# Optimization experiments

Measured on AMD Instinct MI355X. Metric: run time of the kernel, lower is better.

The kernel has to match this reference:

```python
import jax, jax.numpy as jnp
import numpy as np

B, D, N, F = 2048, 512, 100000, 64
NEG = -1000000.0


def setup_inputs() -> dict:
    key = jax.random.key(0)
    k1, k2, k3, k4 = jax.random.split(key, 4)
    q = jax.random.normal(k1, (B, D), dtype=jnp.float32)
    rhs = jax.random.normal(k2, (D, N), dtype=jnp.float32)
    queries = jax.random.randint(k3, (B, 3), 0, N, dtype=jnp.int64)
    filter_idx = jax.random.randint(k4, (B, F), 0, N, dtype=jnp.int64)
    return {"q": q, "rhs": rhs, "queries": queries, "filter_idx": filter_idx}


def reference(q, rhs, queries, filter_idx):
    # targets[i] = score of the true triple = q[i] . rhs[:, true_rhs[i]]
    true_rhs = queries[:, 2]                         # [B]
    targets = jnp.einsum('bd,bd->b', q, rhs[:, true_rhs].T)  # [B]

    scores = q @ rhs                                  # [B, N]

    # filtered ranking: mask out known true tails + the query's own tail
    rows = jnp.arange(scores.shape[0])[:, None]       # [B, 1]
    scores = scores.at[rows, filter_idx].set(NEG)
    scores = scores.at[jnp.arange(scores.shape[0]), true_rhs].set(NEG)

    # rank = 1 + number of candidates scoring >= the true triple
    ranks = 1.0 + jnp.sum((scores >= targets[:, None]).astype(jnp.float32), axis=1)
    return ranks
```

## Files before the change

kernel.cpp:

```cpp
#include <hip/hip_runtime.h>
#include <hip/hip_bf16.h>

#define B_ 2048
#define D_ 512
#define N_ 100000
#define F_ 64
#define NEGV (-1000000.0f)

typedef __bf16 bfx8 __attribute__((ext_vector_type(8)));
typedef float f32x4 __attribute__((ext_vector_type(4)));
typedef unsigned short u16x8 __attribute__((ext_vector_type(8)));

static __device__ __forceinline__ unsigned short f2bf(float f) {
  unsigned u = __float_as_uint(f);
  unsigned r = (u + 0x7fffu + ((u >> 16) & 1u)) >> 16;
  return (unsigned short)r;
}
static __device__ __forceinline__ float bf2f(unsigned short u) {
  return __uint_as_float(((unsigned)u) << 16);
}

static __device__ __forceinline__ void async_copy16(const void* g, void* l) {
  __builtin_amdgcn_global_load_lds((const __attribute__((address_space(1))) void*)g,
                                   (__attribute__((address_space(3))) void*)l, 16, 0, 0);
}

__global__ void targets_convert(const float* __restrict__ q, const float* __restrict__ rhs,
                                const int* __restrict__ queries, float* __restrict__ targets,
                                float* __restrict__ out, unsigned short* __restrict__ qb) {
  __shared__ float wsum[4];
  int b = blockIdx.x;
  int tid = threadIdx.x, lane = tid & 63, w = tid >> 6;
  int p = queries[b * 3 + 2];
  float2 v = ((const float2*)(q + (size_t)b * D_))[tid];
  ushort2 o; o.x = f2bf(v.x); o.y = f2bf(v.y);
  ((ushort2*)(qb + (size_t)b * D_))[tid] = o;
  float s = v.x * rhs[(size_t)(2 * tid) * N_ + p] + v.y * rhs[(size_t)(2 * tid + 1) * N_ + p];
  for (int off = 32; off; off >>= 1) s += __shfl_down(s, off, 64);
  if (lane == 0) wsum[w] = s;
  __syncthreads();
  if (tid == 0) {
    targets[b] = wsum[0] + wsum[1] + wsum[2] + wsum[3];
    out[b] = 1.0f;
  }
}

__global__ void transpose_rhs(const float* __restrict__ rhs, unsigned short* __restrict__ rt) {
  __shared__ float tile[32][260];
  int n0 = blockIdx.x * 256, d0 = blockIdx.y * 32;
  int tid = threadIdx.x;
  if (n0 + 256 <= N_) {
#pragma unroll
    for (int p = 0; p < 8; ++p) {
      int e = p * 256 + tid;
      int d = e >> 6, c4 = e & 63;
      float4 v = *(const float4*)(rhs + (size_t)(d0 + d) * N_ + n0 + c4 * 4);
      *(float4*)&tile[d][c4 * 4] = v;
    }
    __syncthreads();
#pragma unroll
    for (int p = 0; p < 8; ++p) {
      int e = p * 256 + tid;
      int n = e >> 3, dg = e & 7;
      ushort4 o;
      o.x = f2bf(tile[dg * 4 + 0][n]);
      o.y = f2bf(tile[dg * 4 + 1][n]);
      o.z = f2bf(tile[dg * 4 + 2][n]);
      o.w = f2bf(tile[dg * 4 + 3][n]);
      *(ushort4*)(rt + (size_t)(n0 + n) * D_ + d0 + dg * 4) = o;
    }
  } else {
#pragma unroll
    for (int p = 0; p < 8; ++p) {
      int e = p * 256 + tid;
      int d = e >> 6, c4 = e & 63;
      if (n0 + c4 * 4 + 3 < N_) {
        float4 v = *(const float4*)(rhs + (size_t)(d0 + d) * N_ + n0 + c4 * 4);
        *(float4*)&tile[d][c4 * 4] = v;
      }
    }
    __syncthreads();
#pragma unroll
    for (int p = 0; p < 8; ++p) {
      int e = p * 256 + tid;
      int n = e >> 3, dg = e & 7;
      if (n0 + n < N_) {
        ushort4 o;
        o.x = f2bf(tile[dg * 4 + 0][n]);
        o.y = f2bf(tile[dg * 4 + 1][n]);
        o.z = f2bf(tile[dg * 4 + 2][n]);
        o.w = f2bf(tile[dg * 4 + 3][n]);
        *(ushort4*)(rt + (size_t)(n0 + n) * D_ + d0 + dg * 4) = o;
      }
    }
  }
}

__global__ void __launch_bounds__(256) gemm_count(
    const unsigned short* __restrict__ qb,
    const unsigned short* __restrict__ rt,
    const float* __restrict__ targets,
    float* __restrict__ out) {
  __shared__ unsigned short As[2][128 * 32];
  __shared__ unsigned short Bs[2][128 * 32];
  __shared__ float sT[128];
  __shared__ int cnt2[2][128];

  int tid = threadIdx.x;
  int m0 = blockIdx.x * 128;
  int n0 = blockIdx.y * 128;

  if (tid < 128) sT[tid] = targets[m0 + tid];

  int w = tid >> 6, lane = tid & 63;
  int mw = (w & 1) * 64, nw = (w >> 1) * 64;
  int quad = lane >> 4, l16 = lane & 15;

  int c0 = tid, c1 = 256 + tid;
  int am0 = c0 >> 2, aj0 = (c0 & 3) * 8;
  int am1 = c1 >> 2, aj1 = (c1 & 3) * 8;
  int bn0g = n0 + am0; if (bn0g > N_ - 1) bn0g = N_ - 1;
  int bn1g = n0 + am1; if (bn1g > N_ - 1) bn1g = N_ - 1;
  const unsigned short* agp0 = qb + (size_t)(m0 + am0) * D_ + aj0;
  const unsigned short* agp1 = qb + (size_t)(m0 + am1) * D_ + aj1;
  const unsigned short* bgp0 = rt + (size_t)bn0g * D_ + aj0;
  const unsigned short* bgp1 = rt + (size_t)bn1g * D_ + aj1;

  f32x4 acc[4][4];
  f32x4 z = {0.f, 0.f, 0.f, 0.f};
#pragma unroll
  for (int i = 0; i < 4; ++i)
#pragma unroll
    for (int j = 0; j < 4; ++j) acc[i][j] = z;

  async_copy16(agp0, &As[0][c0 * 8]);
  async_copy16(agp1, &As[0][c1 * 8]);
  async_copy16(bgp0, &Bs[0][c0 * 8]);
  async_copy16(bgp1, &Bs[0][c1 * 8]);

  for (int kt = 0; kt < 16; ++kt) {
    int buf = kt & 1;
    __syncthreads();
    if (kt + 1 < 16) {
      int nb = 1 - buf, k1 = (kt + 1) * 32;
      async_copy16(agp0 + k1, &As[nb][c0 * 8]);
      async_copy16(agp1 + k1, &As[nb][c1 * 8]);
      async_copy16(bgp0 + k1, &Bs[nb][c0 * 8]);
      async_copy16(bgp1 + k1, &Bs[nb][c1 * 8]);
    }

    bfx8 a[4], b[4];
#pragma unroll
    for (int mi = 0; mi < 4; ++mi) {
      int m = mw + mi * 16 + l16;
      u16x8 au = *(const u16x8*)(&As[buf][m * 32 + quad * 8]);
      a[mi] = __builtin_bit_cast(bfx8, au);
    }
#pragma unroll
    for (int ni = 0; ni < 4; ++ni) {
      int n = nw + ni * 16 + l16;
      u16x8 bu = *(const u16x8*)(&Bs[buf][n * 32 + quad * 8]);
      b[ni] = __builtin_bit_cast(bfx8, bu);
    }
#pragma unroll
    for (int mi = 0; mi < 4; ++mi)
#pragma unroll
      for (int ni = 0; ni < 4; ++ni)
        acc[mi][ni] = __builtin_amdgcn_mfma_f32_16x16x32_bf16(a[mi], b[ni], acc[mi][ni], 0, 0, 0);
  }

#pragma unroll
  for (int mi = 0; mi < 4; ++mi) {
#pragma unroll
    for (int reg = 0; reg < 4; ++reg) {
      int rl = mw + mi * 16 + quad * 4 + reg;
      float t = sT[rl];
      int c = 0;
#pragma unroll
      for (int ni = 0; ni < 4; ++ni) {
        int col = n0 + nw + ni * 16 + l16;
        if (col < N_ && acc[mi][ni][reg] >= t) c++;
      }
      c += __shfl_xor(c, 1, 64);
      c += __shfl_xor(c, 2, 64);
      c += __shfl_xor(c, 4, 64);
      c += __shfl_xor(c, 8, 64);
      if (l16 == 0) cnt2[w >> 1][rl] = c;
    }
  }
  __syncthreads();
  if (tid < 128) {
    int tot = cnt2[0][tid] + cnt2[1][tid];
    if (tot) atomicAdd(&out[m0 + tid], (float)tot);
  }
}

__global__ void __launch_bounds__(1024) corrections(
    const unsigned short* __restrict__ qb,
    const unsigned short* __restrict__ rt,
    const int* __restrict__ queries,
    const int* __restrict__ filt,
    const float* __restrict__ targets,
    float* __restrict__ out) {
  int b = blockIdx.x;
  int tid = threadIdx.x;
  int w = tid >> 6, lane = tid & 63;
  __shared__ int idx[F_ + 1];
  __shared__ unsigned char uq[F_ + 1];
  if (tid <= F_) idx[tid] = (tid < F_) ? filt[b * F_ + tid] : queries[b * 3 + 2];
  __syncthreads();
  if (tid <= F_) {
    int p = idx[tid];
    bool u = true;
    for (int j = 0; j < tid; ++j)
      if (idx[j] == p) u = false;
    uq[tid] = u;
  }
  __syncthreads();
  float t = targets[b];
  float corr = 0.f;
  u16x8 qv = ((const u16x8*)(qb + (size_t)b * D_))[lane];
  for (int ii = w; ii <= F_; ii += 16) {
    if (!uq[ii]) continue;
    int p = idx[ii];
    u16x8 rv = ((const u16x8*)(rt + (size_t)p * D_))[lane];
    float s = 0.f;
#pragma unroll
    for (int j = 0; j < 8; ++j) s += bf2f(qv[j]) * bf2f(rv[j]);
    for (int off = 32; off; off >>= 1) s += __shfl_down(s, off, 64);
    if (lane == 0)
      corr += (NEGV >= t ? 1.f : 0.f) - (s >= t ? 1.f : 0.f);
  }
  if (lane == 0 && corr != 0.f) atomicAdd(&out[b], corr);
}

__global__ void targets_init(const float* __restrict__ q, const float* __restrict__ rhs,
                             const int* __restrict__ queries, float* __restrict__ targets,
                             float* __restrict__ out) {
  __shared__ float wsum[4];
  int b = blockIdx.x;
  int tid = threadIdx.x, lane = tid & 63, w = tid >> 6;
  int p = queries[b * 3 + 2];
  float s = 0.f;
  for (int d = tid; d < D_; d += 256) s += q[b * D_ + d] * rhs[(size_t)d * N_ + p];
  for (int off = 32; off; off >>= 1) s += __shfl_down(s, off, 64);
  if (lane == 0) wsum[w] = s;
  __syncthreads();
  if (tid == 0) {
    targets[b] = wsum[0] + wsum[1] + wsum[2] + wsum[3];
    out[b] = 1.0f;
  }
}

__global__ void fallback_count(const float* __restrict__ q, const float* __restrict__ rhs,
                               const int* __restrict__ queries, const int* __restrict__ filt,
                               const float* __restrict__ targets, float* __restrict__ out) {
  int b = blockIdx.y;
  int n = blockIdx.x * 256 + threadIdx.x;
  __shared__ float qs[D_];
  __shared__ int idx[F_ + 1];
  __shared__ int cnt;
  for (int d = threadIdx.x; d < D_; d += 256) qs[d] = q[b * D_ + d];
  if (threadIdx.x < F_) idx[threadIdx.x] = filt[b * F_ + threadIdx.x];
  if (threadIdx.x == F_) idx[F_] = queries[b * 3 + 2];
  if (threadIdx.x == 0) cnt = 0;
  __syncthreads();
  if (n < N_) {
    float t = targets[b];
    float s = 0.f;
    for (int d = 0; d < D_; ++d) s += qs[d] * rhs[(size_t)d * N_ + n];
    bool member = false;
    for (int j = 0; j <= F_; ++j)
      if (idx[j] == n) member = true;
    float sv = member ? NEGV : s;
    if (sv >= t) atomicAdd(&cnt, 1);
  }
  __syncthreads();
  if (threadIdx.x == 0 && cnt) atomicAdd(&out[b], (float)cnt);
}

extern "C" void kernel_launch(void* const* d_in, const int* in_sizes, int n_in,
                              void* d_out, int out_size, void* d_ws, size_t ws_size,
                              hipStream_t stream) {
  const float* q = (const float*)d_in[0];
  const float* rhs = (const float*)d_in[1];
  const int* queries = (const int*)d_in[2];
  const int* filt = (const int*)d_in[3];
  float* out = (float*)d_out;

  char* wsb = (char*)d_ws;
  float* targets = (float*)wsb;
  unsigned short* qb = (unsigned short*)(wsb + 8192);
  unsigned short* rt = (unsigned short*)(wsb + 8192 + (size_t)B_ * D_ * 2);
  size_t need = 8192 + (size_t)B_ * D_ * 2 + (size_t)N_ * D_ * 2;

  if (ws_size >= need) {
    targets_convert<<<B_, 256, 0, stream>>>(q, rhs, queries, targets, out, qb);
    transpose_rhs<<<dim3((N_ + 255) / 256, D_ / 32), 256, 0, stream>>>(rhs, rt);
    gemm_count<<<dim3(B_ / 128, (N_ + 127) / 128), 256, 0, stream>>>(qb, rt, targets, out);
    corrections<<<B_, 1024, 0, stream>>>(qb, rt, queries, filt, targets, out);
  } else {
    targets_init<<<B_, 256, 0, stream>>>(q, rhs, queries, targets, out);
    fallback_count<<<dim3((N_ + 255) / 256, B_), 256, 0, stream>>>(q, rhs, queries, filt, targets, out);
  }
}
```

Before: 636.0 us.

## Fuse filter masking into GEMM-count epilogue via per-tile bitmask

Removes the separate corrections kernel and instead builds, per 64x128 output tile, a shared-memory bitmask of filtered and true-tail columns. The GEMM epilogue then skips masked columns when counting. The tile shrinks to 64 rows with 128 threads (2 waves). Each block now scans all 64x64 filter indices for its rows, so every one of the many tiles rereads the filter list, and the smaller blocks halve A reuse per block. One behavioural difference: masked entries are now never counted, whereas the old correction added one count when NEG >= target.

```diff
diff --git a/kernel.cpp b/kernel.cpp
--- a/kernel.cpp
+++ b/kernel.cpp
@@ -15,9 +15,6 @@
   unsigned u = __float_as_uint(f);
   unsigned r = (u + 0x7fffu + ((u >> 16) & 1u)) >> 16;
   return (unsigned short)r;
-}
-static __device__ __forceinline__ float bf2f(unsigned short u) {
-  return __uint_as_float(((unsigned)u) << 16);
 }
 
 static __device__ __forceinline__ void async_copy16(const void* g, void* l) {
@@ -96,142 +93,130 @@
   }
 }
 
-__global__ void __launch_bounds__(256) gemm_count(
-    const unsigned short* __restrict__ qb,
-    const unsigned short* __restrict__ rt,
-    const float* __restrict__ targets,
-    float* __restrict__ out) {
-  __shared__ unsigned short As[2][128 * 32];
-  __shared__ unsigned short Bs[2][128 * 32];
-  __shared__ float sT[128];
-  __shared__ int cnt2[2][128];
-
-  int tid = threadIdx.x;
-  int m0 = blockIdx.x * 128;
-  int n0 = blockIdx.y * 128;
-
-  if (tid < 128) sT[tid] = targets[m0 + tid];
-
-  int w = tid >> 6, lane = tid & 63;
-  int mw = (w & 1) * 64, nw = (w >> 1) * 64;
-  int quad = lane >> 4, l16 = lane & 15;
-
-  int c0 = tid, c1 = 256 + tid;
-  int am0 = c0 >> 2, aj0 = (c0 & 3) * 8;
-  int am1 = c1 >> 2, aj1 = (c1 & 3) * 8;
-  int bn0g = n0 + am0; if (bn0g > N_ - 1) bn0g = N_ - 1;
-  int bn1g = n0 + am1; if (bn1g > N_ - 1) bn1g = N_ - 1;
-  const unsigned short* agp0 = qb + (size_t)(m0 + am0) * D_ + aj0;
-  const unsigned short* agp1 = qb + (size_t)(m0 + am1) * D_ + aj1;
-  const unsigned short* bgp0 = rt + (size_t)bn0g * D_ + aj0;
-  const unsigned short* bgp1 = rt + (size_t)bn1g * D_ + aj1;
-
-  f32x4 acc[4][4];
-  f32x4 z = {0.f, 0.f, 0.f, 0.f};
-#pragma unroll
-  for (int i = 0; i < 4; ++i)
-#pragma unroll
-    for (int j = 0; j < 4; ++j) acc[i][j] = z;
-
-  async_copy16(agp0, &As[0][c0 * 8]);
-  async_copy16(agp1, &As[0][c1 * 8]);
-  async_copy16(bgp0, &Bs[0][c0 * 8]);
-  async_copy16(bgp1, &Bs[0][c1 * 8]);
-
-  for (int kt = 0; kt < 16; ++kt) {
-    int buf = kt & 1;
-    __syncthreads();
-    if (kt + 1 < 16) {
-      int nb = 1 - buf, k1 = (kt + 1) * 32;
-      async_copy16(agp0 + k1, &As[nb][c0 * 8]);
-      async_copy16(agp1 + k1, &As[nb][c1 * 8]);
-      async_copy16(bgp0 + k1, &Bs[nb][c0 * 8]);
-      async_copy16(bgp1 + k1, &Bs[nb][c1 * 8]);
-    }
-
-    bfx8 a[4], b[4];
-#pragma unroll
-    for (int mi = 0; mi < 4; ++mi) {
-      int m = mw + mi * 16 + l16;
-      u16x8 au = *(const u16x8*)(&As[buf][m * 32 + quad * 8]);
-      a[mi] = __builtin_bit_cast(bfx8, au);
-    }
-#pragma unroll
-    for (int ni = 0; ni < 4; ++ni) {
-      int n = nw + ni * 16 + l16;
-      u16x8 bu = *(const u16x8*)(&Bs[buf][n * 32 + quad * 8]);
-      b[ni] = __builtin_bit_cast(bfx8, bu);
-    }
-#pragma unroll
-    for (int mi = 0; mi < 4; ++mi)
-#pragma unroll
-      for (int ni = 0; ni < 4; ++ni)
-        acc[mi][ni] = __builtin_amdgcn_mfma_f32_16x16x32_bf16(a[mi], b[ni], acc[mi][ni], 0, 0, 0);
-  }
-
-#pragma unroll
-  for (int mi = 0; mi < 4; ++mi) {
-#pragma unroll
-    for (int reg = 0; reg < 4; ++reg) {
-      int rl = mw + mi * 16 + quad * 4 + reg;
-      float t = sT[rl];
-      int c = 0;
-#pragma unroll
-      for (int ni = 0; ni < 4; ++ni) {
-        int col = n0 + nw + ni * 16 + l16;
-        if (col < N_ && acc[mi][ni][reg] >= t) c++;
-      }
-      c += __shfl_xor(c, 1, 64);
-      c += __shfl_xor(c, 2, 64);
-      c += __shfl_xor(c, 4, 64);
-      c += __shfl_xor(c, 8, 64);
-      if (l16 == 0) cnt2[w >> 1][rl] = c;
-    }
-  }
-  __syncthreads();
-  if (tid < 128) {
-    int tot = cnt2[0][tid] + cnt2[1][tid];
-    if (tot) atomicAdd(&out[m0 + tid], (float)tot);
-  }
-}
-
-__global__ void __launch_bounds__(1024) corrections(
+__global__ void __launch_bounds__(128) gemm_count(
     const unsigned short* __restrict__ qb,
     const unsigned short* __restrict__ rt,
     const int* __restrict__ queries,
     const int* __restrict__ filt,
     const float* __restrict__ targets,
     float* __restrict__ out) {
-  int b = blockIdx.x;
+  __shared__ unsigned short As[2][64 * 32];
+  __shared__ unsigned short Bs[2][128 * 32];
+  __shared__ float sT[64];
+  __shared__ int cnt2[2][64];
+  __shared__ unsigned bm[64][4];
+
   int tid = threadIdx.x;
+  int m0 = blockIdx.x * 64;
+  int n0 = blockIdx.y * 128;
+
   int w = tid >> 6, lane = tid & 63;
-  __shared__ int idx[F_ + 1];
-  __shared__ unsigned char uq[F_ + 1];
-  if (tid <= F_) idx[tid] = (tid < F_) ? filt[b * F_ + tid] : queries[b * 3 + 2];
-  __syncthreads();
-  if (tid <= F_) {
-    int p = idx[tid];
-    bool u = true;
-    for (int j = 0; j < tid; ++j)
-      if (idx[j] == p) u = false;
-    uq[tid] = u;
-  }
-  __syncthreads();
-  float t = targets[b];
-  float corr = 0.f;
-  u16x8 qv = ((const u16x8*)(qb + (size_t)b * D_))[lane];
-  for (int ii = w; ii <= F_; ii += 16) {
-    if (!uq[ii]) continue;
-    int p = idx[ii];
-    u16x8 rv = ((const u16x8*)(rt + (size_t)p * D_))[lane];
-    float s = 0.f;
-#pragma unroll
-    for (int j = 0; j < 8; ++j) s += bf2f(qv[j]) * bf2f(rv[j]);
-    for (int off = 32; off; off >>= 1) s += __shfl_down(s, off, 64);
-    if (lane == 0)
-      corr += (NEGV >= t ? 1.f : 0.f) - (s >= t ? 1.f : 0.f);
-  }
-  if (lane == 0 && corr != 0.f) atomicAdd(&out[b], corr);
+  int nw = w * 64;
+  int quad = lane >> 4, l16 = lane & 15;
+
+  if (tid < 64) sT[tid] = targets[m0 + tid];
+  ((unsigned*)bm)[tid] = 0;
+  ((unsigned*)bm)[128 + tid] = 0;
+
+  int ca0 = tid, ca1 = 128 + tid;
+  int am0 = ca0 >> 2, aj0 = (ca0 & 3) * 8;
+  int am1 = ca1 >> 2, aj1 = (ca1 & 3) * 8;
+  const unsigned short* agp0 = qb + (size_t)(m0 + am0) * D_ + aj0;
+  const unsigned short* agp1 = qb + (size_t)(m0 + am1) * D_ + aj1;
+  const unsigned short* bgp[4];
+  int cb[4];
+#pragma unroll
+  for (int i = 0; i < 4; ++i) {
+    int c = i * 128 + tid;
+    cb[i] = c;
+    int bn = c >> 2, bj = (c & 3) * 8;
+    int ng = n0 + bn; if (ng > N_ - 1) ng = N_ - 1;
+    bgp[i] = rt + (size_t)ng * D_ + bj;
+  }
+
+  f32x4 acc[4][4];
+  f32x4 z = {0.f, 0.f, 0.f, 0.f};
+#pragma unroll
+  for (int i = 0; i < 4; ++i)
+#pragma unroll
+    for (int j = 0; j < 4; ++j) acc[i][j] = z;
+
+  async_copy16(agp0, &As[0][ca0 * 8]);
+  async_copy16(agp1, &As[0][ca1 * 8]);
+#pragma unroll
+  for (int i = 0; i < 4; ++i) async_copy16(bgp[i], &Bs[0][cb[i] * 8]);
+
+  __syncthreads();
+
+  for (int i = tid; i < 64 * 64; i += 128) {
+    int r = i >> 6, j = i & 63;
+    int p = filt[(size_t)(m0 + r) * 64 + j];
+    unsigned o = (unsigned)(p - n0);
+    if (o < 128u) atomicOr(&bm[r][o >> 5], 1u << (o & 31));
+  }
+  if (tid < 64) {
+    int p = queries[(m0 + tid) * 3 + 2];
+    unsigned o = (unsigned)(p - n0);
+    if (o < 128u) atomicOr(&bm[tid][o >> 5], 1u << (o & 31));
+  }
+
+  for (int kt = 0; kt < 16; ++kt) {
+    int buf = kt & 1;
+    __syncthreads();
+    if (kt + 1 < 16) {
+      int nb = 1 - buf, k1 = (kt + 1) * 32;
+      async_copy16(agp0 + k1, &As[nb][ca0 * 8]);
+      async_copy16(agp1 + k1, &As[nb][ca1 * 8]);
+#pragma unroll
+      for (int i = 0; i < 4; ++i) async_copy16(bgp[i] + k1, &Bs[nb][cb[i] * 8]);
+    }
+
+    bfx8 a[4], b[4];
+#pragma unroll
+    for (int mi = 0; mi < 4; ++mi) {
+      int m = mi * 16 + l16;
+      u16x8 au = *(const u16x8*)(&As[buf][m * 32 + quad * 8]);
+      a[mi] = __builtin_bit_cast(bfx8, au);
+    }
+#pragma unroll
+    for (int ni = 0; ni < 4; ++ni) {
+      int n = nw + ni * 16 + l16;
+      u16x8 bu = *(const u16x8*)(&Bs[buf][n * 32 + quad * 8]);
+      b[ni] = __builtin_bit_cast(bfx8, bu);
+    }
+#pragma unroll
+    for (int mi = 0; mi < 4; ++mi)
+#pragma unroll
+      for (int ni = 0; ni < 4; ++ni)
+        acc[mi][ni] = __builtin_amdgcn_mfma_f32_16x16x32_bf16(a[mi], b[ni], acc[mi][ni], 0, 0, 0);
+  }
+
+#pragma unroll
+  for (int mi = 0; mi < 4; ++mi) {
+#pragma unroll
+    for (int reg = 0; reg < 4; ++reg) {
+      int rl = mi * 16 + quad * 4 + reg;
+      float t = sT[rl];
+      unsigned long long bmv = *(const unsigned long long*)&bm[rl][w * 2];
+      int c = 0;
+#pragma unroll
+      for (int ni = 0; ni < 4; ++ni) {
+        int o = ni * 16 + l16;
+        int col = n0 + nw + o;
+        if (col < N_ && !((bmv >> o) & 1ull) && acc[mi][ni][reg] >= t) c++;
+      }
+      c += __shfl_xor(c, 1, 64);
+      c += __shfl_xor(c, 2, 64);
+      c += __shfl_xor(c, 4, 64);
+      c += __shfl_xor(c, 8, 64);
+      if (l16 == 0) cnt2[w][rl] = c;
+    }
+  }
+  __syncthreads();
+  if (tid < 64) {
+    int tot = cnt2[0][tid] + cnt2[1][tid];
+    if (tot) atomicAdd(&out[m0 + tid], (float)tot);
+  }
 }
 
 __global__ void targets_init(const float* __restrict__ q, const float* __restrict__ rhs,
@@ -297,8 +282,7 @@
   if (ws_size >= need) {
     targets_convert<<<B_, 256, 0, stream>>>(q, rhs, queries, targets, out, qb);
     transpose_rhs<<<dim3((N_ + 255) / 256, D_ / 32), 256, 0, stream>>>(rhs, rt);
-    gemm_count<<<dim3(B_ / 128, (N_ + 127) / 128), 256, 0, stream>>>(qb, rt, targets, out);
-    corrections<<<B_, 1024, 0, stream>>>(qb, rt, queries, filt, targets, out);
+    gemm_count<<<dim3(B_ / 64, (N_ + 127) / 128), 128, 0, stream>>>(qb, rt, queries, filt, targets, out);
   } else {
     targets_init<<<B_, 256, 0, stream>>>(q, rhs, queries, targets, out);
     fallback_count<<<dim3((N_ + 255) / 256, B_), 256, 0, stream>>>(q, rhs, queries, filt, targets, out);
```

Result: slower. 798.5 us (+25.6%).

## Fuse filter masking into GEMM count via shared bitmask and swizzle tile order

Applied to the files above, without the earlier changes.

Removes the separate corrections kernel. Each GEMM tile now builds a per-row shared-memory bitmask of filtered and true-tail columns that fall inside its 128-column range, and skips those columns when counting scores at or above the target. The grid becomes 1D with a grouped mapping, so 8 neighbouring N-tiles run across all 16 M-tiles, which is meant to improve L2 reuse of the rhs tiles. The cost is that every block reads the full 128x64 filter slab for its M-tile and runs a pre-loop shared-atomic pass, which adds traffic and latency ahead of the MFMA loop.

```diff
diff --git a/kernel.cpp b/kernel.cpp
--- a/kernel.cpp
+++ b/kernel.cpp
@@ -6,6 +6,7 @@
 #define N_ 100000
 #define F_ 64
 #define NEGV (-1000000.0f)
+#define NT_ 782
 
 typedef __bf16 bfx8 __attribute__((ext_vector_type(8)));
 typedef float f32x4 __attribute__((ext_vector_type(4)));
@@ -15,9 +16,6 @@
   unsigned u = __float_as_uint(f);
   unsigned r = (u + 0x7fffu + ((u >> 16) & 1u)) >> 16;
   return (unsigned short)r;
-}
-static __device__ __forceinline__ float bf2f(unsigned short u) {
-  return __uint_as_float(((unsigned)u) << 16);
 }
 
 static __device__ __forceinline__ void async_copy16(const void* g, void* l) {
@@ -99,18 +97,29 @@
 __global__ void __launch_bounds__(256) gemm_count(
     const unsigned short* __restrict__ qb,
     const unsigned short* __restrict__ rt,
+    const int* __restrict__ queries,
+    const int* __restrict__ filt,
     const float* __restrict__ targets,
     float* __restrict__ out) {
   __shared__ unsigned short As[2][128 * 32];
   __shared__ unsigned short Bs[2][128 * 32];
   __shared__ float sT[128];
   __shared__ int cnt2[2][128];
+  __shared__ unsigned bm[128][4];
+
+  unsigned bid = blockIdx.x;
+  int c = bid & 7;
+  unsigned s = bid >> 3;
+  int m = s & 15, j = s >> 4;
+  int nt = j * 8 + c;
+  if (nt >= NT_) return;
+  int m0 = m * 128;
+  int n0 = nt * 128;
 
   int tid = threadIdx.x;
-  int m0 = blockIdx.x * 128;
-  int n0 = blockIdx.y * 128;
-
   if (tid < 128) sT[tid] = targets[m0 + tid];
+  ((unsigned*)bm)[tid] = 0;
+  ((unsigned*)bm)[256 + tid] = 0;
 
   int w = tid >> 6, lane = tid & 63;
   int mw = (w & 1) * 64, nw = (w >> 1) * 64;
@@ -131,12 +140,26 @@
 #pragma unroll
   for (int i = 0; i < 4; ++i)
 #pragma unroll
-    for (int j = 0; j < 4; ++j) acc[i][j] = z;
+    for (int jq = 0; jq < 4; ++jq) acc[i][jq] = z;
 
   async_copy16(agp0, &As[0][c0 * 8]);
   async_copy16(agp1, &As[0][c1 * 8]);
   async_copy16(bgp0, &Bs[0][c0 * 8]);
   async_copy16(bgp1, &Bs[0][c1 * 8]);
+
+  __syncthreads();
+
+  for (int i = tid; i < 128 * 64; i += 256) {
+    int r = i >> 6, f = i & 63;
+    int p = filt[(size_t)(m0 + r) * 64 + f];
+    unsigned o = (unsigned)(p - n0);
+    if (o < 128u) atomicOr(&bm[r][o >> 5], 1u << (o & 31));
+  }
+  if (tid < 128) {
+    int p = queries[(m0 + tid) * 3 + 2];
+    unsigned o = (unsigned)(p - n0);
+    if (o < 128u) atomicOr(&bm[tid][o >> 5], 1u << (o & 31));
+  }
 
   for (int kt = 0; kt < 16; ++kt) {
     int buf = kt & 1;
@@ -152,14 +175,14 @@
     bfx8 a[4], b[4];
 #pragma unroll
     for (int mi = 0; mi < 4; ++mi) {
-      int m = mw + mi * 16 + l16;
-      u16x8 au = *(const u16x8*)(&As[buf][m * 32 + quad * 8]);
+      int mm = mw + mi * 16 + l16;
+      u16x8 au = *(const u16x8*)(&As[buf][mm * 32 + quad * 8]);
       a[mi] = __builtin_bit_cast(bfx8, au);
     }
 #pragma unroll
     for (int ni = 0; ni < 4; ++ni) {
-      int n = nw + ni * 16 + l16;
-      u16x8 bu = *(const u16x8*)(&Bs[buf][n * 32 + quad * 8]);
+      int nn = nw + ni * 16 + l16;
+      u16x8 bu = *(const u16x8*)(&Bs[buf][nn * 32 + quad * 8]);
       b[ni] = __builtin_bit_cast(bfx8, bu);
     }
 #pragma unroll
@@ -175,17 +198,19 @@
     for (int reg = 0; reg < 4; ++reg) {
       int rl = mw + mi * 16 + quad * 4 + reg;
       float t = sT[rl];
-      int c = 0;
+      unsigned long long bmv = *(const unsigned long long*)&bm[rl][nw >> 5];
+      int cc = 0;
 #pragma unroll
       for (int ni = 0; ni < 4; ++ni) {
-        int col = n0 + nw + ni * 16 + l16;
-        if (col < N_ && acc[mi][ni][reg] >= t) c++;
+        int o = ni * 16 + l16;
+        int col = n0 + nw + o;
+        if (col < N_ && !((bmv >> o) & 1ull) && acc[mi][ni][reg] >= t) cc++;
       }
-      c += __shfl_xor(c, 1, 64);
-      c += __shfl_xor(c, 2, 64);
-      c += __shfl_xor(c, 4, 64);
-      c += __shfl_xor(c, 8, 64);
-      if (l16 == 0) cnt2[w >> 1][rl] = c;
+      cc += __shfl_xor(cc, 1, 64);
+      cc += __shfl_xor(cc, 2, 64);
+      cc += __shfl_xor(cc, 4, 64);
+      cc += __shfl_xor(cc, 8, 64);
+      if (l16 == 0) cnt2[w >> 1][rl] = cc;
     }
   }
   __syncthreads();
@@ -193,45 +218,6 @@
     int tot = cnt2[0][tid] + cnt2[1][tid];
     if (tot) atomicAdd(&out[m0 + tid], (float)tot);
   }
-}
-
-__global__ void __launch_bounds__(1024) corrections(
-    const unsigned short* __restrict__ qb,
-    const unsigned short* __restrict__ rt,
-    const int* __restrict__ queries,
-    const int* __restrict__ filt,
-    const float* __restrict__ targets,
-    float* __restrict__ out) {
-  int b = blockIdx.x;
-  int tid = threadIdx.x;
-  int w = tid >> 6, lane = tid & 63;
-  __shared__ int idx[F_ + 1];
-  __shared__ unsigned char uq[F_ + 1];
-  if (tid <= F_) idx[tid] = (tid < F_) ? filt[b * F_ + tid] : queries[b * 3 + 2];
-  __syncthreads();
-  if (tid <= F_) {
-    int p = idx[tid];
-    bool u = true;
-    for (int j = 0; j < tid; ++j)
-      if (idx[j] == p) u = false;
-    uq[tid] = u;
-  }
-  __syncthreads();
-  float t = targets[b];
-  float corr = 0.f;
-  u16x8 qv = ((const u16x8*)(qb + (size_t)b * D_))[lane];
-  for (int ii = w; ii <= F_; ii += 16) {
-    if (!uq[ii]) continue;
-    int p = idx[ii];
-    u16x8 rv = ((const u16x8*)(rt + (size_t)p * D_))[lane];
-    float s = 0.f;
-#pragma unroll
-    for (int j = 0; j < 8; ++j) s += bf2f(qv[j]) * bf2f(rv[j]);
-    for (int off = 32; off; off >>= 1) s += __shfl_down(s, off, 64);
-    if (lane == 0)
-      corr += (NEGV >= t ? 1.f : 0.f) - (s >= t ? 1.f : 0.f);
-  }
-  if (lane == 0 && corr != 0.f) atomicAdd(&out[b], corr);
 }
 
 __global__ void targets_init(const float* __restrict__ q, const float* __restrict__ rhs,
@@ -297,8 +283,7 @@
   if (ws_size >= need) {
     targets_convert<<<B_, 256, 0, stream>>>(q, rhs, queries, targets, out, qb);
     transpose_rhs<<<dim3((N_ + 255) / 256, D_ / 32), 256, 0, stream>>>(rhs, rt);
-    gemm_count<<<dim3(B_ / 128, (N_ + 127) / 128), 256, 0, stream>>>(qb, rt, targets, out);
-    corrections<<<B_, 1024, 0, stream>>>(qb, rt, queries, filt, targets, out);
+    gemm_count<<<8 * 16 * 98, 256, 0, stream>>>(qb, rt, queries, filt, targets, out);
   } else {
     targets_init<<<B_, 256, 0, stream>>>(q, rhs, queries, targets, out);
     fallback_count<<<dim3((N_ + 255) / 256, B_), 256, 0, stream>>>(q, rhs, queries, filt, targets, out);
```

New measurement: 722.2 us. 1.14x slower.
